# Optimization experiments

Hardware: AMD Instinct MI355X
Metric: run time of the kernel (lower is better)

The kernel has to match this reference:

```python
import jax, jax.numpy as jnp
import numpy as np

DIM = 768
H = 12
DH = DIM // H          # 64
ROPE_DIM = (DH // 6) * 6   # 60
HALF = (ROPE_DIM // 3) // 2  # 10 freqs per axis
THETA = 10000.0
EPS = 1e-6


def rmsnorm(x, w):
    xf = x.astype(jnp.float32)
    var = jnp.mean(xf * xf, axis=-1, keepdims=True)
    return (w * (xf * jax.lax.rsqrt(var + EPS))).astype(x.dtype)


def rope_angles(positions):
    # positions: [B, N, 3] -> angles [B, N, 3*HALF]
    freqs = 1.0 / (THETA ** (jnp.arange(HALF, dtype=jnp.float32) / HALF))  # [HALF]
    # [B,N,3,1] * [1,1,1,HALF] -> [B,N,3,HALF] -> concat over axis order x,y,z
    ang = positions[..., :, None] * freqs[None, None, None, :]
    return ang.reshape(*positions.shape[:2], 3 * HALF)  # [B,N,30]


def apply_rope(t, cos, sin):
    # t: [B,N,H,ROPE_DIM]; cos/sin: [B,N,1,ROPE_DIM//2]
    B, N, Hh, D = t.shape
    tf = t.astype(jnp.float32).reshape(B, N, Hh, D // 2, 2)
    te, to = tf[..., 0], tf[..., 1]
    oe = te * cos - to * sin
    oo = te * sin + to * cos
    return jnp.stack([oe, oo], axis=-1).reshape(B, N, Hh, D).astype(t.dtype)


def setup_inputs() -> dict:
    key = jax.random.key(0)
    ks = jax.random.split(key, 5)
    B, N = 2, 2048
    x = jax.random.normal(ks[0], (B, N, DIM), dtype=jnp.float32)
    positions = jax.random.uniform(ks[1], (B, N, 3), dtype=jnp.float32)
    qkv_w = jax.random.normal(ks[2], (3 * DIM, DIM), dtype=jnp.float32) * (DIM ** -0.5)
    proj_w = jax.random.normal(ks[3], (DIM, DIM), dtype=jnp.float32) * (DIM ** -0.5)
    proj_b = jnp.zeros((DIM,), dtype=jnp.float32)
    qn_w = jnp.ones((DH,), dtype=jnp.float32)
    kn_w = jnp.ones((DH,), dtype=jnp.float32)
    return {"x": x, "positions": positions, "qkv_w": qkv_w, "proj_w": proj_w,
            "proj_b": proj_b, "qn_w": qn_w, "kn_w": kn_w}


def reference(x, positions, qkv_w, proj_w, proj_b, qn_w, kn_w):
    B, N, C = x.shape
    scale = DH ** -0.5
    qkv = (x @ qkv_w.T).reshape(B, N, 3, H, DH)
    q, k, v = qkv[:, :, 0], qkv[:, :, 1], qkv[:, :, 2]  # [B,N,H,DH]
    q = rmsnorm(q, qn_w)
    k = rmsnorm(k, kn_w)
    # 3D RoPE on first ROPE_DIM channels
    ang = rope_angles(positions)                 # [B,N,30]
    cos = jnp.cos(ang)[:, :, None, :]            # [B,N,1,30]
    sin = jnp.sin(ang)[:, :, None, :]
    q = jnp.concatenate([apply_rope(q[..., :ROPE_DIM], cos, sin), q[..., ROPE_DIM:]], axis=-1)
    k = jnp.concatenate([apply_rope(k[..., :ROPE_DIM], cos, sin), k[..., ROPE_DIM:]], axis=-1)
    attn = jnp.einsum('bqhd,bkhd->bhqk', q, k) * scale  # [B,H,N,N]
    attn = jax.nn.softmax(attn, axis=-1)
    out = jnp.einsum('bhqk,bkhd->bqhd', attn, v).reshape(B, N, C)
    return out @ proj_w.T + proj_b
```

## Files before the change

### kernel.cpp

```cpp
#include <hip/hip_runtime.h>
#include <hip/hip_bf16.h>
#include <math.h>

#define DIM 768
#define NH 12
#define DH 64
#define SEQ 2048
#define BATCH 2
#define TOK (BATCH*SEQ)
#define QKVN (3*DIM)

typedef __attribute__((ext_vector_type(8))) short bf16x8;
typedef __attribute__((ext_vector_type(4))) float f32x4;
typedef __attribute__((ext_vector_type(2))) unsigned int u32x2;
typedef unsigned short u16;

#define VM0 asm volatile("s_waitcnt vmcnt(0)" ::: "memory")
#define VM3 asm volatile("s_waitcnt vmcnt(3)" ::: "memory")
#define VM4 asm volatile("s_waitcnt vmcnt(4)" ::: "memory")
#define LGKM0 asm volatile("s_waitcnt lgkmcnt(0)" ::: "memory")
#define BAR() __builtin_amdgcn_s_barrier()

__device__ inline u16 f2bf(float f) {
  union { float f; unsigned u; } v; v.f = f;
  unsigned u = v.u;
  u += 0x7fffu + ((u >> 16) & 1u);
  return (u16)(u >> 16);
}

__device__ inline int pkbf(float a, float b) {
  __hip_bfloat162 h = __float22bfloat162_rn(make_float2(a, b));
  int r; __builtin_memcpy(&r, &h, 4); return r;
}

__global__ void conv_all(const float* __restrict__ a, u16* __restrict__ ao, int na4,
                         const float* __restrict__ b, u16* __restrict__ bo, int nb4,
                         const float* __restrict__ c, u16* __restrict__ co, int nc4,
                         const float* __restrict__ pos, float2* __restrict__ tab) {
  int i4 = blockIdx.x * blockDim.x + threadIdx.x;
  const int nconv = na4 + nb4 + nc4;
  if (i4 < nconv) {
    const float* src; u16* dst; int off;
    if (i4 < na4)            { src = a; dst = ao; off = i4; }
    else if (i4 < na4 + nb4) { src = b; dst = bo; off = i4 - na4; }
    else                     { src = c; dst = co; off = i4 - na4 - nb4; }
    float4 v = ((const float4*)src)[off];
    ushort4 o;
    o.x = f2bf(v.x); o.y = f2bf(v.y); o.z = f2bf(v.z); o.w = f2bf(v.w);
    ((ushort4*)dst)[off] = o;
    return;
  }
  int e = i4 - nconv;
  if (e >= TOK * 32) return;
  int t = e >> 5, p = e & 31;
  float cs = 1.f, sn = 0.f;
  if (p < 30) {
    int axis = p / 10, fi = p % 10;
    float freq = exp2f(-(float)fi * 1.3287712379549449f);
    float ang = pos[t * 3 + axis] * freq;
    cs = cosf(ang); sn = sinf(ang);
  }
  tab[e] = make_float2(cs, sn);
}

#define GLL(g, s) __builtin_amdgcn_global_load_lds((const __attribute__((address_space(1))) void*)(g), (__attribute__((address_space(3))) void*)(s), 16, 0, 0)

__global__ __launch_bounds__(256, 4) void gemm64(
    const u16* __restrict__ A, const u16* __restrict__ W,
    float* __restrict__ C, const float* __restrict__ bias,
    int M, int Nn, int K)
{
  __shared__ u16 As[2][64 * 64];
  __shared__ u16 Bs[2][64 * 64];
  const int t = threadIdx.x;
  const int w = t >> 6, l = t & 63;
  const int lr = l & 15, lg = l >> 4;
  const int wr = w >> 1, wc = w & 1;
  const int m0 = blockIdx.x * 64;
  const int n0 = blockIdx.y * 64;
  f32x4 acc[2][2] = {};
  const int srow = t >> 3;
  const int scol = (((t & 7) ^ (srow & 7)) * 8);
  const u16* aSrc = A + (size_t)(m0 + srow) * K + scol;
  const u16* bSrc = W + (size_t)(n0 + srow) * K + scol;
  const size_t r32 = (size_t)32 * K;
  const int sw = lr & 7;
  const int NT = K / 64;

  GLL(aSrc,       &As[0][w * 512]);
  GLL(aSrc + r32, &As[0][2048 + w * 512]);
  GLL(bSrc,       &Bs[0][w * 512]);
  GLL(bSrc + r32, &Bs[0][2048 + w * 512]);

  for (int kt = 0; kt < NT; ++kt) {
    const int cur = kt & 1;
    if (kt + 1 < NT) {
      const int k0 = (kt + 1) * 64;
      GLL(aSrc + k0,       &As[cur ^ 1][w * 512]);
      GLL(aSrc + r32 + k0, &As[cur ^ 1][2048 + w * 512]);
      GLL(bSrc + k0,       &Bs[cur ^ 1][w * 512]);
      GLL(bSrc + r32 + k0, &Bs[cur ^ 1][2048 + w * 512]);
      VM4;
    } else {
      VM0;
    }
    BAR();
#pragma unroll
    for (int kk = 0; kk < 2; ++kk) {
      bf16x8 af[2], bff[2];
#pragma unroll
      for (int mi = 0; mi < 2; ++mi)
        af[mi] = *(const bf16x8*)(&As[cur][0] + (wr * 32 + mi * 16 + lr) * 64 + (((kk * 4 + lg) ^ sw) * 8));
#pragma unroll
      for (int ni = 0; ni < 2; ++ni)
        bff[ni] = *(const bf16x8*)(&Bs[cur][0] + (wc * 32 + ni * 16 + lr) * 64 + (((kk * 4 + lg) ^ sw) * 8));
#pragma unroll
      for (int mi = 0; mi < 2; ++mi)
#pragma unroll
        for (int ni = 0; ni < 2; ++ni)
          acc[mi][ni] = __builtin_amdgcn_mfma_f32_16x16x32_bf16(af[mi], bff[ni], acc[mi][ni], 0, 0, 0);
    }
    LGKM0;
    BAR();
  }

#pragma unroll
  for (int mi = 0; mi < 2; ++mi)
#pragma unroll
    for (int ni = 0; ni < 2; ++ni)
#pragma unroll
      for (int r = 0; r < 4; ++r) {
        int row = m0 + wr * 32 + mi * 16 + lg * 4 + r;
        int col = n0 + wc * 32 + ni * 16 + lr;
        C[(size_t)row * Nn + col] = acc[mi][ni][r] + bias[col];
      }
}

__global__ __launch_bounds__(512, 6) void gemm_qkv(
    const u16* __restrict__ A, const u16* __restrict__ W,
    const float* __restrict__ qn_w, const float* __restrict__ kn_w,
    const float2* __restrict__ tab,
    u16* __restrict__ Qb, u16* __restrict__ Kb, u16* __restrict__ Vtb)
{
  __shared__ u16 As[2][128 * 64];
  __shared__ u16 Bs[2][64 * 64];
  const int K = DIM;
  const int t = threadIdx.x;
  const int w = t >> 6, l = t & 63;
  const int lr = l & 15, lg = l >> 4;
  const int m0 = blockIdx.x * 128;
  const int n0 = blockIdx.y * 64;
  f32x4 acc[4] = {};
  const int srow = t >> 3;
  const int scol = (((t & 7) ^ (srow & 7)) * 8);
  const u16* aSrc = A + (size_t)(m0 + srow) * K + scol;
  const u16* bSrc = W + (size_t)(n0 + srow) * K + scol;
  const size_t r64 = (size_t)64 * K;
  const int sw = lr & 7;
  const int NT = K / 64;

  GLL(aSrc,       &As[0][w * 512]);
  GLL(aSrc + r64, &As[0][4096 + w * 512]);
  GLL(bSrc,       &Bs[0][w * 512]);

  for (int kt = 0; kt < NT; ++kt) {
    const int cur = kt & 1;
    if (kt + 1 < NT) {
      const int k0 = (kt + 1) * 64;
      GLL(aSrc + k0,       &As[cur ^ 1][w * 512]);
      GLL(aSrc + r64 + k0, &As[cur ^ 1][4096 + w * 512]);
      GLL(bSrc + k0,       &Bs[cur ^ 1][w * 512]);
      VM3;
    } else {
      VM0;
    }
    BAR();
#pragma unroll
    for (int kk = 0; kk < 2; ++kk) {
      bf16x8 af = *(const bf16x8*)(&As[cur][0] + (w * 16 + lr) * 64 + (((kk * 4 + lg) ^ sw) * 8));
      bf16x8 bff[4];
#pragma unroll
      for (int ni = 0; ni < 4; ++ni)
        bff[ni] = *(const bf16x8*)(&Bs[cur][0] + (ni * 16 + lr) * 64 + (((kk * 4 + lg) ^ sw) * 8));
#pragma unroll
      for (int ni = 0; ni < 4; ++ni)
        acc[ni] = __builtin_amdgcn_mfma_f32_16x16x32_bf16(af, bff[ni], acc[ni], 0, 0, 0);
    }
    LGKM0;
    BAR();
  }

  const int chunk = n0 >> 6;
  const int tt = chunk / 12;
  const int h  = chunk % 12;
  const int bB = m0 >> 11;
  const int bh = bB * NH + h;

  if (tt == 2) {
    const int nbase = (m0 + w * 16 + lg * 4) & 2047;
#pragma unroll
    for (int ni = 0; ni < 4; ++ni) {
      const int d = ni * 16 + lr;
      ushort4 o;
      o.x = f2bf(acc[ni][0]); o.y = f2bf(acc[ni][1]);
      o.z = f2bf(acc[ni][2]); o.w = f2bf(acc[ni][3]);
      *(ushort4*)(Vtb + ((size_t)bh * DH + d) * SEQ + nbase) = o;
    }
  } else {
    const float* wv = (tt == 0 ? qn_w : kn_w);
    const float qs = (tt == 0 ? 0.125f * 1.4426950408889634f : 1.f);
    float wgt[4];
#pragma unroll
    for (int ni = 0; ni < 4; ++ni) wgt[ni] = wv[ni * 16 + lr];
    u16* outp = (tt == 0 ? Qb : Kb) + (size_t)bh * SEQ * DH;
#pragma unroll
    for (int r = 0; r < 4; ++r) {
      float ss = 0.f;
#pragma unroll
      for (int ni = 0; ni < 4; ++ni) ss += acc[ni][r] * acc[ni][r];
      ss += __shfl_xor(ss, 1, 64);
      ss += __shfl_xor(ss, 2, 64);
      ss += __shfl_xor(ss, 4, 64);
      ss += __shfl_xor(ss, 8, 64);
      const float rms = rsqrtf(ss * (1.f / 64.f) + 1e-6f);
      const int trow = m0 + w * 16 + lg * 4 + r;
      const float2* tl = tab + trow * 32;
      u16* rowp = outp + (size_t)(trow & 2047) * DH;
#pragma unroll
      for (int ni = 0; ni < 4; ++ni) {
        const int d = ni * 16 + lr;
        float v = acc[ni][r] * rms * wgt[ni];
        float vp = __shfl_xor(v, 1, 64);
        float2 cssn = tl[ni * 8 + (lr >> 1)];
        float sgn = (d & 1) ? cssn.y : -cssn.y;
        rowp[d] = f2bf((v * cssn.x + vp * sgn) * qs);
      }
    }
  }
}

__global__ __launch_bounds__(256, 3) void attn(
    const u16* __restrict__ Qb, const u16* __restrict__ Kb,
    const u16* __restrict__ Vtb, u16* __restrict__ Ob)
{
  __shared__ u16 Ks[2][2][64 * 64];
  __shared__ u16 Vs[2][64 * 64];
  const int tid = threadIdx.x;
  const int w = tid >> 6, l = tid & 63;
  const int lr = l & 15, lg = l >> 4;
  const int qg = w & 1, half = w >> 1;
  const int wg = blockIdx.x;
  const int swz = (wg & 7) * 96 + (wg >> 3);
  const int bh = swz >> 5;
  const int q0 = (swz & 31) * 64;
  const u16* Qp = Qb + (size_t)bh * SEQ * DH;
  const u16* Kp = Kb + (size_t)bh * SEQ * DH;
  const u16* Vp = Vtb + (size_t)bh * DH * SEQ;

  const int qrA = q0 + qg * 32 + lr;
  const bf16x8 bq0a = *(const bf16x8*)(Qp + (size_t)qrA * DH + 8 * lg);
  const bf16x8 bq1a = *(const bf16x8*)(Qp + (size_t)qrA * DH + 32 + 8 * lg);
  const bf16x8 bq0b = *(const bf16x8*)(Qp + (size_t)(qrA + 16) * DH + 8 * lg);
  const bf16x8 bq1b = *(const bf16x8*)(Qp + (size_t)(qrA + 16) * DH + 32 + 8 * lg);

  const int srow = tid >> 3;
  const int sc16 = (tid & 7) ^ (srow & 7);
  const u16* kSrc = Kp + (size_t)srow * DH + sc16 * 8;
  const u16* vSrc = Vp + (size_t)srow * SEQ + sc16 * 8;

  const int frow = (lr & 3) | ((lr & 4) << 1) | ((lr & 8) >> 1);
  const int ksw = frow & 7;
  const int vsw = lr & 7;

  bf16x8 vone;
#pragma unroll
  for (int j = 0; j < 8; ++j) vone[j] = (short)0x3F80;

  f32x4 oaccA[4] = {}, oaccB[4] = {};
  f32x4 laccA = {}, laccB = {};

  GLL(kSrc,          &Ks[0][0][w * 512]);
  GLL(kSrc + 2048,   &Ks[0][0][w * 512 + 2048]);
  GLL(kSrc + 4096,   &Ks[0][1][w * 512]);
  GLL(kSrc + 6144,   &Ks[0][1][w * 512 + 2048]);
  VM0;
  BAR();
  GLL(vSrc,              &Vs[0][w * 512]);
  GLL(vSrc + 65536,      &Vs[0][w * 512 + 2048]);
  GLL(vSrc + 64,         &Vs[1][w * 512]);
  GLL(vSrc + 64 + 65536, &Vs[1][w * 512 + 2048]);
  GLL(kSrc + 8192,   &Ks[1][0][w * 512]);
  GLL(kSrc + 10240,  &Ks[1][0][w * 512 + 2048]);
  GLL(kSrc + 12288,  &Ks[1][1][w * 512]);
  GLL(kSrc + 14336,  &Ks[1][1][w * 512 + 2048]);

  for (int i = 0; i < 16; ++i) {
    const int p = i & 1;
    const u16* Kt = &Ks[p][half][0];
    const u16* Vt = &Vs[half][0];

    f32x4 paccA[4] = {}, paccB[4] = {};
    __builtin_amdgcn_s_setprio(1);
#pragma unroll
    for (int c = 0; c < 4; ++c) {
      const int rbase = (16 * c + frow) * 64;
      bf16x8 ka = *(const bf16x8*)(Kt + rbase + ((lg ^ ksw) * 8));
      bf16x8 kb = *(const bf16x8*)(Kt + rbase + (((4 + lg) ^ ksw) * 8));
      paccA[c] = __builtin_amdgcn_mfma_f32_16x16x32_bf16(ka, bq0a, paccA[c], 0, 0, 0);
      paccA[c] = __builtin_amdgcn_mfma_f32_16x16x32_bf16(kb, bq1a, paccA[c], 0, 0, 0);
      paccB[c] = __builtin_amdgcn_mfma_f32_16x16x32_bf16(ka, bq0b, paccB[c], 0, 0, 0);
      paccB[c] = __builtin_amdgcn_mfma_f32_16x16x32_bf16(kb, bq1b, paccB[c], 0, 0, 0);
    }
    __builtin_amdgcn_s_setprio(0);

    union { unsigned d[4]; bf16x8 v; } puA[2], puB[2];
#pragma unroll
    for (int g = 0; g < 2; ++g) {
      const int clo = 2 * g, chi = 2 * g + 1;
      float eA[8], eB[8];
#pragma unroll
      for (int r = 0; r < 4; ++r) {
        eA[r]     = __builtin_amdgcn_exp2f(paccA[clo][r]);
        eA[4 + r] = __builtin_amdgcn_exp2f(paccA[chi][r]);
        eB[r]     = __builtin_amdgcn_exp2f(paccB[clo][r]);
        eB[4 + r] = __builtin_amdgcn_exp2f(paccB[chi][r]);
      }
      u32x2 a0 = __builtin_amdgcn_permlane32_swap((unsigned)pkbf(eA[0], eA[1]),
                                                  (unsigned)pkbf(eA[4], eA[5]), false, false);
      u32x2 a1 = __builtin_amdgcn_permlane32_swap((unsigned)pkbf(eA[2], eA[3]),
                                                  (unsigned)pkbf(eA[6], eA[7]), false, false);
      u32x2 b0 = __builtin_amdgcn_permlane32_swap((unsigned)pkbf(eB[0], eB[1]),
                                                  (unsigned)pkbf(eB[4], eB[5]), false, false);
      u32x2 b1 = __builtin_amdgcn_permlane32_swap((unsigned)pkbf(eB[2], eB[3]),
                                                  (unsigned)pkbf(eB[6], eB[7]), false, false);
      puA[g].d[0] = a0[0]; puA[g].d[1] = a1[0]; puA[g].d[2] = a0[1]; puA[g].d[3] = a1[1];
      puB[g].d[0] = b0[0]; puB[g].d[1] = b1[0]; puB[g].d[2] = b0[1]; puB[g].d[3] = b1[1];
    }

    if (i < 15) { VM4; } else { VM0; }
    BAR();

    __builtin_amdgcn_s_setprio(1);
#pragma unroll
    for (int g = 0; g < 2; ++g) {
#pragma unroll
      for (int dt = 0; dt < 4; ++dt) {
        bf16x8 va = *(const bf16x8*)(Vt + (16 * dt + lr) * 64 + (((4 * g + lg) ^ vsw) * 8));
        oaccA[dt] = __builtin_amdgcn_mfma_f32_16x16x32_bf16(va, puA[g].v, oaccA[dt], 0, 0, 0);
        oaccB[dt] = __builtin_amdgcn_mfma_f32_16x16x32_bf16(va, puB[g].v, oaccB[dt], 0, 0, 0);
      }
      laccA = __builtin_amdgcn_mfma_f32_16x16x32_bf16(vone, puA[g].v, laccA, 0, 0, 0);
      laccB = __builtin_amdgcn_mfma_f32_16x16x32_bf16(vone, puB[g].v, laccB, 0, 0, 0);
    }
    __builtin_amdgcn_s_setprio(0);

    LGKM0;
    VM0;
    BAR();

    if (i + 1 < 16) {
      const size_t vo = (size_t)(2 * i + 2) * 64;
      GLL(vSrc + vo,              &Vs[0][w * 512]);
      GLL(vSrc + vo + 65536,      &Vs[0][w * 512 + 2048]);
      GLL(vSrc + vo + 64,         &Vs[1][w * 512]);
      GLL(vSrc + vo + 64 + 65536, &Vs[1][w * 512 + 2048]);
    }
    if (i + 2 < 16) {
      const size_t ko = (size_t)(2 * i + 4) * 4096;
      GLL(kSrc + ko,        &Ks[p][0][w * 512]);
      GLL(kSrc + ko + 2048, &Ks[p][0][w * 512 + 2048]);
      GLL(kSrc + ko + 4096, &Ks[p][1][w * 512]);
      GLL(kSrc + ko + 6144, &Ks[p][1][w * 512 + 2048]);
    }
  }

  float* scr = (float*)&Ks[0][0][0];
  const int sidA = (qg * 2 + 0) * 64 + l;
  const int sidB = (qg * 2 + 1) * 64 + l;
  if (half == 1) {
#pragma unroll
    for (int dt = 0; dt < 4; ++dt)
#pragma unroll
      for (int r = 0; r < 4; ++r) {
        scr[sidA * 17 + dt * 4 + r] = oaccA[dt][r];
        scr[sidB * 17 + dt * 4 + r] = oaccB[dt][r];
      }
    scr[sidA * 17 + 16] = laccA[0];
    scr[sidB * 17 + 16] = laccB[0];
  }
  __syncthreads();
  if (half == 1) return;
#pragma unroll
  for (int dt = 0; dt < 4; ++dt)
#pragma unroll
    for (int r = 0; r < 4; ++r) {
      oaccA[dt][r] += scr[sidA * 17 + dt * 4 + r];
      oaccB[dt][r] += scr[sidB * 17 + dt * 4 + r];
    }
  const float invA = 1.f / (laccA[0] + scr[sidA * 17 + 16]);
  const float invB = 1.f / (laccB[0] + scr[sidB * 17 + 16]);

  const int b = bh / NH, h = bh % NH;
  const int qA = q0 + qg * 32 + lr;
  size_t obA = (size_t)(b * SEQ + qA) * DIM + h * DH + 4 * lg;
  size_t obB = (size_t)(b * SEQ + qA + 16) * DIM + h * DH + 4 * lg;
#pragma unroll
  for (int dt = 0; dt < 4; ++dt) {
    ushort4 oA, oB;
    oA.x = f2bf(oaccA[dt][0] * invA); oA.y = f2bf(oaccA[dt][1] * invA);
    oA.z = f2bf(oaccA[dt][2] * invA); oA.w = f2bf(oaccA[dt][3] * invA);
    oB.x = f2bf(oaccB[dt][0] * invB); oB.y = f2bf(oaccB[dt][1] * invB);
    oB.z = f2bf(oaccB[dt][2] * invB); oB.w = f2bf(oaccB[dt][3] * invB);
    *(ushort4*)(Ob + obA + 16 * dt) = oA;
    *(ushort4*)(Ob + obB + 16 * dt) = oB;
  }
}

extern "C" void kernel_launch(void* const* d_in, const int* in_sizes, int n_in,
                              void* d_out, int out_size, void* d_ws, size_t ws_size,
                              hipStream_t stream) {
  const float* x      = (const float*)d_in[0];
  const float* pos    = (const float*)d_in[1];
  const float* qkv_w  = (const float*)d_in[2];
  const float* proj_w = (const float*)d_in[3];
  const float* proj_b = (const float*)d_in[4];
  const float* qn_w   = (const float*)d_in[5];
  const float* kn_w   = (const float*)d_in[6];
  char* ws = (char*)d_ws;
  u16*    xb    = (u16*)(ws + 0);
  u16*    wqkv  = (u16*)(ws + 6291456);
  u16*    wproj = (u16*)(ws + 9830400);
  float2* tab   = (float2*)(ws + 11010048);
  u16*    Qb    = (u16*)(ws + 12058624);
  u16*    Kb    = (u16*)(ws + 18350080);
  u16*    Vtb   = (u16*)(ws + 24641536);
  u16*    Ob    = (u16*)(ws + 30932992);
  float* out = (float*)d_out;

  const int na4 = TOK * DIM / 4, nb4 = QKVN * DIM / 4, nc4 = DIM * DIM / 4;
  const int ntot = na4 + nb4 + nc4 + TOK * 32;
  conv_all<<<(ntot + 255) / 256, 256, 0, stream>>>(
      x, xb, na4, qkv_w, wqkv, nb4, proj_w, wproj, nc4, pos, tab);

  dim3 g1(TOK / 128, QKVN / 64);
  gemm_qkv<<<g1, 512, 0, stream>>>(xb, wqkv, qn_w, kn_w, tab, Qb, Kb, Vtb);

  attn<<<SEQ / 64 * BATCH * NH, 256, 0, stream>>>(Qb, Kb, Vtb, Ob);

  dim3 g3(TOK / 64, DIM / 64);
  gemm64<<<g3, 256, 0, stream>>>(Ob, wproj, out, proj_b, TOK, DIM, DIM);
}
```

Before: 87.12 us.

## Fuse fp32-to-bf16 conversion and RoPE table into GEMM loaders

Removes the separate conversion kernel. The QKV and projection GEMMs now load fp32 inputs and weights directly through registers, convert them to bf16 and write them into swizzled LDS, which replaces the async global-to-LDS path. The RoPE cos/sin values are computed inline in the QKV epilogue from the positions instead of read from a precomputed table. This saves one launch and the bf16 round trip through memory, but doubles the bytes each GEMM reads, re-converts weights in every block, and adds transcendental work to the epilogue.

```diff
diff --git a/kernel.cpp b/kernel.cpp
--- a/kernel.cpp
+++ b/kernel.cpp
@@ -16,7 +16,6 @@
 typedef unsigned short u16;
 
 #define VM0 asm volatile("s_waitcnt vmcnt(0)" ::: "memory")
-#define VM3 asm volatile("s_waitcnt vmcnt(3)" ::: "memory")
 #define VM4 asm volatile("s_waitcnt vmcnt(4)" ::: "memory")
 #define LGKM0 asm volatile("s_waitcnt lgkmcnt(0)" ::: "memory")
 #define BAR() __builtin_amdgcn_s_barrier()
@@ -33,40 +32,17 @@
   int r; __builtin_memcpy(&r, &h, 4); return r;
 }
 
-__global__ void conv_all(const float* __restrict__ a, u16* __restrict__ ao, int na4,
-                         const float* __restrict__ b, u16* __restrict__ bo, int nb4,
-                         const float* __restrict__ c, u16* __restrict__ co, int nc4,
-                         const float* __restrict__ pos, float2* __restrict__ tab) {
-  int i4 = blockIdx.x * blockDim.x + threadIdx.x;
-  const int nconv = na4 + nb4 + nc4;
-  if (i4 < nconv) {
-    const float* src; u16* dst; int off;
-    if (i4 < na4)            { src = a; dst = ao; off = i4; }
-    else if (i4 < na4 + nb4) { src = b; dst = bo; off = i4 - na4; }
-    else                     { src = c; dst = co; off = i4 - na4 - nb4; }
-    float4 v = ((const float4*)src)[off];
-    ushort4 o;
-    o.x = f2bf(v.x); o.y = f2bf(v.y); o.z = f2bf(v.z); o.w = f2bf(v.w);
-    ((ushort4*)dst)[off] = o;
-    return;
-  }
-  int e = i4 - nconv;
-  if (e >= TOK * 32) return;
-  int t = e >> 5, p = e & 31;
-  float cs = 1.f, sn = 0.f;
-  if (p < 30) {
-    int axis = p / 10, fi = p % 10;
-    float freq = exp2f(-(float)fi * 1.3287712379549449f);
-    float ang = pos[t * 3 + axis] * freq;
-    cs = cosf(ang); sn = sinf(ang);
-  }
-  tab[e] = make_float2(cs, sn);
+__device__ inline void wr8(u16* dst, float4 x, float4 y) {
+  union { u16 u[8]; bf16x8 v; } o;
+  o.u[0] = f2bf(x.x); o.u[1] = f2bf(x.y); o.u[2] = f2bf(x.z); o.u[3] = f2bf(x.w);
+  o.u[4] = f2bf(y.x); o.u[5] = f2bf(y.y); o.u[6] = f2bf(y.z); o.u[7] = f2bf(y.w);
+  *(bf16x8*)dst = o.v;
 }
 
 #define GLL(g, s) __builtin_amdgcn_global_load_lds((const __attribute__((address_space(1))) void*)(g), (__attribute__((address_space(3))) void*)(s), 16, 0, 0)
 
 __global__ __launch_bounds__(256, 4) void gemm64(
-    const u16* __restrict__ A, const u16* __restrict__ W,
+    const u16* __restrict__ A, const float* __restrict__ W,
     float* __restrict__ C, const float* __restrict__ bias,
     int M, int Nn, int K)
 {
@@ -80,31 +56,42 @@
   const int n0 = blockIdx.y * 64;
   f32x4 acc[2][2] = {};
   const int srow = t >> 3;
-  const int scol = (((t & 7) ^ (srow & 7)) * 8);
-  const u16* aSrc = A + (size_t)(m0 + srow) * K + scol;
-  const u16* bSrc = W + (size_t)(n0 + srow) * K + scol;
+  const int sc16 = (t & 7) ^ (srow & 7);
+  const u16* aSrc = A + (size_t)(m0 + srow) * K + sc16 * 8;
   const size_t r32 = (size_t)32 * K;
+  const int rw = t >> 2, jw = (t & 3) * 2;
+  const float* bSrc = W + (size_t)(n0 + rw) * K + jw * 8;
+  const int wof0 = rw * 64 + ((jw ^ (rw & 7)) * 8);
+  const int wof1 = rw * 64 + (((jw + 1) ^ (rw & 7)) * 8);
   const int sw = lr & 7;
   const int NT = K / 64;
 
   GLL(aSrc,       &As[0][w * 512]);
   GLL(aSrc + r32, &As[0][2048 + w * 512]);
-  GLL(bSrc,       &Bs[0][w * 512]);
-  GLL(bSrc + r32, &Bs[0][2048 + w * 512]);
+  {
+    float4 b0 = *(const float4*)(bSrc);
+    float4 b1 = *(const float4*)(bSrc + 4);
+    float4 b2 = *(const float4*)(bSrc + 8);
+    float4 b3 = *(const float4*)(bSrc + 12);
+    wr8(&Bs[0][wof0], b0, b1);
+    wr8(&Bs[0][wof1], b2, b3);
+  }
+  VM0; LGKM0; BAR();
 
   for (int kt = 0; kt < NT; ++kt) {
     const int cur = kt & 1;
-    if (kt + 1 < NT) {
+    const bool pre = (kt + 1 < NT);
+    float4 b0, b1, b2, b3;
+    if (pre) {
       const int k0 = (kt + 1) * 64;
       GLL(aSrc + k0,       &As[cur ^ 1][w * 512]);
       GLL(aSrc + r32 + k0, &As[cur ^ 1][2048 + w * 512]);
-      GLL(bSrc + k0,       &Bs[cur ^ 1][w * 512]);
-      GLL(bSrc + r32 + k0, &Bs[cur ^ 1][2048 + w * 512]);
-      VM4;
-    } else {
-      VM0;
-    }
-    BAR();
+      const float* bp = bSrc + k0;
+      b0 = *(const float4*)(bp);
+      b1 = *(const float4*)(bp + 4);
+      b2 = *(const float4*)(bp + 8);
+      b3 = *(const float4*)(bp + 12);
+    }
 #pragma unroll
     for (int kk = 0; kk < 2; ++kk) {
       bf16x8 af[2], bff[2];
@@ -120,7 +107,12 @@
         for (int ni = 0; ni < 2; ++ni)
           acc[mi][ni] = __builtin_amdgcn_mfma_f32_16x16x32_bf16(af[mi], bff[ni], acc[mi][ni], 0, 0, 0);
     }
+    if (pre) {
+      wr8(&Bs[cur ^ 1][wof0], b0, b1);
+      wr8(&Bs[cur ^ 1][wof1], b2, b3);
+    }
     LGKM0;
+    VM0;
     BAR();
   }
 
@@ -137,9 +129,9 @@
 }
 
 __global__ __launch_bounds__(512, 6) void gemm_qkv(
-    const u16* __restrict__ A, const u16* __restrict__ W,
+    const float* __restrict__ X, const float* __restrict__ Wq,
     const float* __restrict__ qn_w, const float* __restrict__ kn_w,
-    const float2* __restrict__ tab,
+    const float* __restrict__ pos,
     u16* __restrict__ Qb, u16* __restrict__ Kb, u16* __restrict__ Vtb)
 {
   __shared__ u16 As[2][128 * 64];
@@ -151,30 +143,43 @@
   const int m0 = blockIdx.x * 128;
   const int n0 = blockIdx.y * 64;
   f32x4 acc[4] = {};
-  const int srow = t >> 3;
-  const int scol = (((t & 7) ^ (srow & 7)) * 8);
-  const u16* aSrc = A + (size_t)(m0 + srow) * K + scol;
-  const u16* bSrc = W + (size_t)(n0 + srow) * K + scol;
-  const size_t r64 = (size_t)64 * K;
+  const int ra = t >> 2, ja = (t & 3) * 2;
+  const float* aSrc = X + (size_t)(m0 + ra) * K + ja * 8;
+  const int aof0 = ra * 64 + ((ja ^ (ra & 7)) * 8);
+  const int aof1 = ra * 64 + (((ja + 1) ^ (ra & 7)) * 8);
+  const int rb = t >> 3, jb = t & 7;
+  const float* bSrc = Wq + (size_t)(n0 + rb) * K + jb * 8;
+  const int bof = rb * 64 + ((jb ^ (rb & 7)) * 8);
   const int sw = lr & 7;
   const int NT = K / 64;
 
-  GLL(aSrc,       &As[0][w * 512]);
-  GLL(aSrc + r64, &As[0][4096 + w * 512]);
-  GLL(bSrc,       &Bs[0][w * 512]);
+  {
+    float4 a0 = *(const float4*)(aSrc);
+    float4 a1 = *(const float4*)(aSrc + 4);
+    float4 a2 = *(const float4*)(aSrc + 8);
+    float4 a3 = *(const float4*)(aSrc + 12);
+    float4 b0 = *(const float4*)(bSrc);
+    float4 b1 = *(const float4*)(bSrc + 4);
+    wr8(&As[0][aof0], a0, a1);
+    wr8(&As[0][aof1], a2, a3);
+    wr8(&Bs[0][bof], b0, b1);
+  }
+  LGKM0; BAR();
 
   for (int kt = 0; kt < NT; ++kt) {
     const int cur = kt & 1;
-    if (kt + 1 < NT) {
-      const int k0 = (kt + 1) * 64;
-      GLL(aSrc + k0,       &As[cur ^ 1][w * 512]);
-      GLL(aSrc + r64 + k0, &As[cur ^ 1][4096 + w * 512]);
-      GLL(bSrc + k0,       &Bs[cur ^ 1][w * 512]);
-      VM3;
-    } else {
-      VM0;
-    }
-    BAR();
+    const bool pre = (kt + 1 < NT);
+    float4 a0, a1, a2, a3, b0, b1;
+    if (pre) {
+      const float* ap = aSrc + (kt + 1) * 64;
+      const float* bp = bSrc + (kt + 1) * 64;
+      a0 = *(const float4*)(ap);
+      a1 = *(const float4*)(ap + 4);
+      a2 = *(const float4*)(ap + 8);
+      a3 = *(const float4*)(ap + 12);
+      b0 = *(const float4*)(bp);
+      b1 = *(const float4*)(bp + 4);
+    }
 #pragma unroll
     for (int kk = 0; kk < 2; ++kk) {
       bf16x8 af = *(const bf16x8*)(&As[cur][0] + (w * 16 + lr) * 64 + (((kk * 4 + lg) ^ sw) * 8));
@@ -185,6 +190,11 @@
 #pragma unroll
       for (int ni = 0; ni < 4; ++ni)
         acc[ni] = __builtin_amdgcn_mfma_f32_16x16x32_bf16(af, bff[ni], acc[ni], 0, 0, 0);
+    }
+    if (pre) {
+      wr8(&As[cur ^ 1][aof0], a0, a1);
+      wr8(&As[cur ^ 1][aof1], a2, a3);
+      wr8(&Bs[cur ^ 1][bof], b0, b1);
     }
     LGKM0;
     BAR();
@@ -209,9 +219,17 @@
   } else {
     const float* wv = (tt == 0 ? qn_w : kn_w);
     const float qs = (tt == 0 ? 0.125f * 1.4426950408889634f : 1.f);
-    float wgt[4];
-#pragma unroll
-    for (int ni = 0; ni < 4; ++ni) wgt[ni] = wv[ni * 16 + lr];
+    float wgt[4], freqv[4];
+    int axv[4]; bool actv[4];
+#pragma unroll
+    for (int ni = 0; ni < 4; ++ni) {
+      wgt[ni] = wv[ni * 16 + lr];
+      const int pidx = ni * 8 + (lr >> 1);
+      actv[ni] = (pidx < 30);
+      const int axis = pidx / 10, fi = pidx % 10;
+      axv[ni] = axis;
+      freqv[ni] = exp2f(-(float)fi * 1.3287712379549449f);
+    }
     u16* outp = (tt == 0 ? Qb : Kb) + (size_t)bh * SEQ * DH;
 #pragma unroll
     for (int r = 0; r < 4; ++r) {
@@ -224,16 +242,21 @@
       ss += __shfl_xor(ss, 8, 64);
       const float rms = rsqrtf(ss * (1.f / 64.f) + 1e-6f);
       const int trow = m0 + w * 16 + lg * 4 + r;
-      const float2* tl = tab + trow * 32;
+      const float pa = pos[trow * 3], pb = pos[trow * 3 + 1], pc = pos[trow * 3 + 2];
       u16* rowp = outp + (size_t)(trow & 2047) * DH;
 #pragma unroll
       for (int ni = 0; ni < 4; ++ni) {
         const int d = ni * 16 + lr;
+        float cs = 1.f, sn = 0.f;
+        if (actv[ni]) {
+          const float pv = (axv[ni] == 0) ? pa : ((axv[ni] == 1) ? pb : pc);
+          const float ang = pv * freqv[ni];
+          cs = cosf(ang); sn = sinf(ang);
+        }
         float v = acc[ni][r] * rms * wgt[ni];
         float vp = __shfl_xor(v, 1, 64);
-        float2 cssn = tl[ni * 8 + (lr >> 1)];
-        float sgn = (d & 1) ? cssn.y : -cssn.y;
-        rowp[d] = f2bf((v * cssn.x + vp * sgn) * qs);
+        float sgn = (d & 1) ? sn : -sn;
+        rowp[d] = f2bf((v * cs + vp * sgn) * qs);
       }
     }
   }
@@ -427,26 +450,17 @@
   const float* qn_w   = (const float*)d_in[5];
   const float* kn_w   = (const float*)d_in[6];
   char* ws = (char*)d_ws;
-  u16*    xb    = (u16*)(ws + 0);
-  u16*    wqkv  = (u16*)(ws + 6291456);
-  u16*    wproj = (u16*)(ws + 9830400);
-  float2* tab   = (float2*)(ws + 11010048);
-  u16*    Qb    = (u16*)(ws + 12058624);
-  u16*    Kb    = (u16*)(ws + 18350080);
-  u16*    Vtb   = (u16*)(ws + 24641536);
-  u16*    Ob    = (u16*)(ws + 30932992);
+  u16* Qb  = (u16*)(ws + 0);
+  u16* Kb  = (u16*)(ws + 6291456);
+  u16* Vtb = (u16*)(ws + 12582912);
+  u16* Ob  = (u16*)(ws + 18874368);
   float* out = (float*)d_out;
 
-  const int na4 = TOK * DIM / 4, nb4 = QKVN * DIM / 4, nc4 = DIM * DIM / 4;
-  const int ntot = na4 + nb4 + nc4 + TOK * 32;
-  conv_all<<<(ntot + 255) / 256, 256, 0, stream>>>(
-      x, xb, na4, qkv_w, wqkv, nb4, proj_w, wproj, nc4, pos, tab);
-
   dim3 g1(TOK / 128, QKVN / 64);
-  gemm_qkv<<<g1, 512, 0, stream>>>(xb, wqkv, qn_w, kn_w, tab, Qb, Kb, Vtb);
+  gemm_qkv<<<g1, 512, 0, stream>>>(x, qkv_w, qn_w, kn_w, pos, Qb, Kb, Vtb);
 
   attn<<<SEQ / 64 * BATCH * NH, 256, 0, stream>>>(Qb, Kb, Vtb, Ob);
 
   dim3 g3(TOK / 64, DIM / 64);
-  gemm64<<<g3, 256, 0, stream>>>(Ob, wproj, out, proj_b, TOK, DIM, DIM);
-}
+  gemm64<<<g3, 256, 0, stream>>>(Ob, proj_w, out, proj_b, TOK, DIM, DIM);
+}
```

Result: slower. 107.5 us (+23.4%).

## Give each attention wave 16 queries over all keys instead of split-key halves

Applied to the files above, without the earlier changes.

The attention kernel changes its work split. Before, each wave handled 32 queries over half of every key/value tile, and the two halves were reduced through shared memory at the end. Now each wave owns 16 query rows over the full key range, using a simple two-stage double buffer of 64-key K/V tiles with one barrier per iteration. This removes the cross-wave reduction and cuts shared memory from 48KB to 32KB, and launch bounds rise from 3 to 5 blocks for higher occupancy. In exchange, each K/V fragment read from shared memory now feeds half as many MFMAs, and the loop runs twice as many iterations and barriers.

```diff
diff --git a/kernel.cpp b/kernel.cpp
--- a/kernel.cpp
+++ b/kernel.cpp
@@ -239,16 +239,15 @@
   }
 }
 
-__global__ __launch_bounds__(256, 3) void attn(
+__global__ __launch_bounds__(256, 5) void attn(
     const u16* __restrict__ Qb, const u16* __restrict__ Kb,
     const u16* __restrict__ Vtb, u16* __restrict__ Ob)
 {
-  __shared__ u16 Ks[2][2][64 * 64];
-  __shared__ u16 Vs[2][64 * 64];
+  __shared__ u16 Kd[2][64 * 64];
+  __shared__ u16 Vd[2][64 * 64];
   const int tid = threadIdx.x;
   const int w = tid >> 6, l = tid & 63;
   const int lr = l & 15, lg = l >> 4;
-  const int qg = w & 1, half = w >> 1;
   const int wg = blockIdx.x;
   const int swz = (wg & 7) * 96 + (wg >> 3);
   const int bh = swz >> 5;
@@ -257,11 +256,9 @@
   const u16* Kp = Kb + (size_t)bh * SEQ * DH;
   const u16* Vp = Vtb + (size_t)bh * DH * SEQ;
 
-  const int qrA = q0 + qg * 32 + lr;
-  const bf16x8 bq0a = *(const bf16x8*)(Qp + (size_t)qrA * DH + 8 * lg);
-  const bf16x8 bq1a = *(const bf16x8*)(Qp + (size_t)qrA * DH + 32 + 8 * lg);
-  const bf16x8 bq0b = *(const bf16x8*)(Qp + (size_t)(qrA + 16) * DH + 8 * lg);
-  const bf16x8 bq1b = *(const bf16x8*)(Qp + (size_t)(qrA + 16) * DH + 32 + 8 * lg);
+  const int qrow = q0 + w * 16 + lr;
+  const bf16x8 bq0 = *(const bf16x8*)(Qp + (size_t)qrow * DH + 8 * lg);
+  const bf16x8 bq1 = *(const bf16x8*)(Qp + (size_t)qrow * DH + 32 + 8 * lg);
 
   const int srow = tid >> 3;
   const int sc16 = (tid & 7) ^ (srow & 7);
@@ -276,69 +273,57 @@
 #pragma unroll
   for (int j = 0; j < 8; ++j) vone[j] = (short)0x3F80;
 
-  f32x4 oaccA[4] = {}, oaccB[4] = {};
-  f32x4 laccA = {}, laccB = {};
-
-  GLL(kSrc,          &Ks[0][0][w * 512]);
-  GLL(kSrc + 2048,   &Ks[0][0][w * 512 + 2048]);
-  GLL(kSrc + 4096,   &Ks[0][1][w * 512]);
-  GLL(kSrc + 6144,   &Ks[0][1][w * 512 + 2048]);
+  f32x4 oacc[4] = {};
+  f32x4 lacc = {};
+
+  GLL(kSrc,         &Kd[0][w * 512]);
+  GLL(kSrc + 2048,  &Kd[0][w * 512 + 2048]);
+  GLL(vSrc,         &Vd[0][w * 512]);
+  GLL(vSrc + 65536, &Vd[0][w * 512 + 2048]);
   VM0;
   BAR();
-  GLL(vSrc,              &Vs[0][w * 512]);
-  GLL(vSrc + 65536,      &Vs[0][w * 512 + 2048]);
-  GLL(vSrc + 64,         &Vs[1][w * 512]);
-  GLL(vSrc + 64 + 65536, &Vs[1][w * 512 + 2048]);
-  GLL(kSrc + 8192,   &Ks[1][0][w * 512]);
-  GLL(kSrc + 10240,  &Ks[1][0][w * 512 + 2048]);
-  GLL(kSrc + 12288,  &Ks[1][1][w * 512]);
-  GLL(kSrc + 14336,  &Ks[1][1][w * 512 + 2048]);
-
-  for (int i = 0; i < 16; ++i) {
-    const int p = i & 1;
-    const u16* Kt = &Ks[p][half][0];
-    const u16* Vt = &Vs[half][0];
-
-    f32x4 paccA[4] = {}, paccB[4] = {};
+
+  for (int i = 0; i < 32; ++i) {
+    const int cur = i & 1;
+    if (i + 1 < 32) {
+      const size_t ko = (size_t)(i + 1) * 4096;
+      const size_t vo = (size_t)(i + 1) * 64;
+      GLL(kSrc + ko,         &Kd[cur ^ 1][w * 512]);
+      GLL(kSrc + ko + 2048,  &Kd[cur ^ 1][w * 512 + 2048]);
+      GLL(vSrc + vo,         &Vd[cur ^ 1][w * 512]);
+      GLL(vSrc + vo + 65536, &Vd[cur ^ 1][w * 512 + 2048]);
+    }
+    const u16* Kt = &Kd[cur][0];
+    const u16* Vt = &Vd[cur][0];
+
+    f32x4 pacc[4] = {};
     __builtin_amdgcn_s_setprio(1);
 #pragma unroll
     for (int c = 0; c < 4; ++c) {
       const int rbase = (16 * c + frow) * 64;
       bf16x8 ka = *(const bf16x8*)(Kt + rbase + ((lg ^ ksw) * 8));
       bf16x8 kb = *(const bf16x8*)(Kt + rbase + (((4 + lg) ^ ksw) * 8));
-      paccA[c] = __builtin_amdgcn_mfma_f32_16x16x32_bf16(ka, bq0a, paccA[c], 0, 0, 0);
-      paccA[c] = __builtin_amdgcn_mfma_f32_16x16x32_bf16(kb, bq1a, paccA[c], 0, 0, 0);
-      paccB[c] = __builtin_amdgcn_mfma_f32_16x16x32_bf16(ka, bq0b, paccB[c], 0, 0, 0);
-      paccB[c] = __builtin_amdgcn_mfma_f32_16x16x32_bf16(kb, bq1b, paccB[c], 0, 0, 0);
+      pacc[c] = __builtin_amdgcn_mfma_f32_16x16x32_bf16(ka, bq0, pacc[c], 0, 0, 0);
+      pacc[c] = __builtin_amdgcn_mfma_f32_16x16x32_bf16(kb, bq1, pacc[c], 0, 0, 0);
     }
     __builtin_amdgcn_s_setprio(0);
 
-    union { unsigned d[4]; bf16x8 v; } puA[2], puB[2];
+    union { unsigned d[4]; bf16x8 v; } pu[2];
 #pragma unroll
     for (int g = 0; g < 2; ++g) {
       const int clo = 2 * g, chi = 2 * g + 1;
-      float eA[8], eB[8];
+      float e[8];
 #pragma unroll
       for (int r = 0; r < 4; ++r) {
-        eA[r]     = __builtin_amdgcn_exp2f(paccA[clo][r]);
-        eA[4 + r] = __builtin_amdgcn_exp2f(paccA[chi][r]);
-        eB[r]     = __builtin_amdgcn_exp2f(paccB[clo][r]);
-        eB[4 + r] = __builtin_amdgcn_exp2f(paccB[chi][r]);
+        e[r]     = __builtin_amdgcn_exp2f(pacc[clo][r]);
+        e[4 + r] = __builtin_amdgcn_exp2f(pacc[chi][r]);
       }
-      u32x2 a0 = __builtin_amdgcn_permlane32_swap((unsigned)pkbf(eA[0], eA[1]),
-                                                  (unsigned)pkbf(eA[4], eA[5]), false, false);
-      u32x2 a1 = __builtin_amdgcn_permlane32_swap((unsigned)pkbf(eA[2], eA[3]),
-                                                  (unsigned)pkbf(eA[6], eA[7]), false, false);
-      u32x2 b0 = __builtin_amdgcn_permlane32_swap((unsigned)pkbf(eB[0], eB[1]),
-                                                  (unsigned)pkbf(eB[4], eB[5]), false, false);
-      u32x2 b1 = __builtin_amdgcn_permlane32_swap((unsigned)pkbf(eB[2], eB[3]),
-                                                  (unsigned)pkbf(eB[6], eB[7]), false, false);
-      puA[g].d[0] = a0[0]; puA[g].d[1] = a1[0]; puA[g].d[2] = a0[1]; puA[g].d[3] = a1[1];
-      puB[g].d[0] = b0[0]; puB[g].d[1] = b1[0]; puB[g].d[2] = b0[1]; puB[g].d[3] = b1[1];
-    }
-
-    if (i < 15) { VM4; } else { VM0; }
-    BAR();
+      u32x2 a0 = __builtin_amdgcn_permlane32_swap((unsigned)pkbf(e[0], e[1]),
+                                                  (unsigned)pkbf(e[4], e[5]), false, false);
+      u32x2 a1 = __builtin_amdgcn_permlane32_swap((unsigned)pkbf(e[2], e[3]),
+                                                  (unsigned)pkbf(e[6], e[7]), false, false);
+      pu[g].d[0] = a0[0]; pu[g].d[1] = a1[0]; pu[g].d[2] = a0[1]; pu[g].d[3] = a1[1];
+    }
 
     __builtin_amdgcn_s_setprio(1);
 #pragma unroll
@@ -346,73 +331,31 @@
 #pragma unroll
       for (int dt = 0; dt < 4; ++dt) {
         bf16x8 va = *(const bf16x8*)(Vt + (16 * dt + lr) * 64 + (((4 * g + lg) ^ vsw) * 8));
-        oaccA[dt] = __builtin_amdgcn_mfma_f32_16x16x32_bf16(va, puA[g].v, oaccA[dt], 0, 0, 0);
-        oaccB[dt] = __builtin_amdgcn_mfma_f32_16x16x32_bf16(va, puB[g].v, oaccB[dt], 0, 0, 0);
+        oacc[dt] = __builtin_amdgcn_mfma_f32_16x16x32_bf16(va, pu[g].v, oacc[dt], 0, 0, 0);
       }
-      laccA = __builtin_amdgcn_mfma_f32_16x16x32_bf16(vone, puA[g].v, laccA, 0, 0, 0);
-      laccB = __builtin_amdgcn_mfma_f32_16x16x32_bf16(vone, puB[g].v, laccB, 0, 0, 0);
+      lacc = __builtin_amdgcn_mfma_f32_16x16x32_bf16(vone, pu[g].v, lacc, 0, 0, 0);
     }
     __builtin_amdgcn_s_setprio(0);
 
-    LGKM0;
-    VM0;
-    BAR();
-
-    if (i + 1 < 16) {
-      const size_t vo = (size_t)(2 * i + 2) * 64;
-      GLL(vSrc + vo,              &Vs[0][w * 512]);
-      GLL(vSrc + vo + 65536,      &Vs[0][w * 512 + 2048]);
-      GLL(vSrc + vo + 64,         &Vs[1][w * 512]);
-      GLL(vSrc + vo + 64 + 65536, &Vs[1][w * 512 + 2048]);
-    }
-    if (i + 2 < 16) {
-      const size_t ko = (size_t)(2 * i + 4) * 4096;
-      GLL(kSrc + ko,        &Ks[p][0][w * 512]);
-      GLL(kSrc + ko + 2048, &Ks[p][0][w * 512 + 2048]);
-      GLL(kSrc + ko + 4096, &Ks[p][1][w * 512]);
-      GLL(kSrc + ko + 6144, &Ks[p][1][w * 512 + 2048]);
-    }
-  }
-
-  float* scr = (float*)&Ks[0][0][0];
-  const int sidA = (qg * 2 + 0) * 64 + l;
-  const int sidB = (qg * 2 + 1) * 64 + l;
-  if (half == 1) {
-#pragma unroll
-    for (int dt = 0; dt < 4; ++dt)
-#pragma unroll
-      for (int r = 0; r < 4; ++r) {
-        scr[sidA * 17 + dt * 4 + r] = oaccA[dt][r];
-        scr[sidB * 17 + dt * 4 + r] = oaccB[dt][r];
-      }
-    scr[sidA * 17 + 16] = laccA[0];
-    scr[sidB * 17 + 16] = laccB[0];
-  }
-  __syncthreads();
-  if (half == 1) return;
-#pragma unroll
-  for (int dt = 0; dt < 4; ++dt)
-#pragma unroll
-    for (int r = 0; r < 4; ++r) {
-      oaccA[dt][r] += scr[sidA * 17 + dt * 4 + r];
-      oaccB[dt][r] += scr[sidB * 17 + dt * 4 + r];
-    }
-  const float invA = 1.f / (laccA[0] + scr[sidA * 17 + 16]);
-  const float invB = 1.f / (laccB[0] + scr[sidB * 17 + 16]);
-
+    if (i + 1 < 32) {
+      LGKM0;
+      VM0;
+      BAR();
+    }
+  }
+
+  const float inv = 1.f / lacc[0];
   const int b = bh / NH, h = bh % NH;
-  const int qA = q0 + qg * 32 + lr;
-  size_t obA = (size_t)(b * SEQ + qA) * DIM + h * DH + 4 * lg;
-  size_t obB = (size_t)(b * SEQ + qA + 16) * DIM + h * DH + 4 * lg;
+  const int q = q0 + w * 16 + lr;
+  size_t obase = (size_t)(b * SEQ + q) * DIM + h * DH + 4 * lg;
 #pragma unroll
   for (int dt = 0; dt < 4; ++dt) {
-    ushort4 oA, oB;
-    oA.x = f2bf(oaccA[dt][0] * invA); oA.y = f2bf(oaccA[dt][1] * invA);
-    oA.z = f2bf(oaccA[dt][2] * invA); oA.w = f2bf(oaccA[dt][3] * invA);
-    oB.x = f2bf(oaccB[dt][0] * invB); oB.y = f2bf(oaccB[dt][1] * invB);
-    oB.z = f2bf(oaccB[dt][2] * invB); oB.w = f2bf(oaccB[dt][3] * invB);
-    *(ushort4*)(Ob + obA + 16 * dt) = oA;
-    *(ushort4*)(Ob + obB + 16 * dt) = oB;
+    ushort4 o;
+    o.x = f2bf(oacc[dt][0] * inv);
+    o.y = f2bf(oacc[dt][1] * inv);
+    o.z = f2bf(oacc[dt][2] * inv);
+    o.w = f2bf(oacc[dt][3] * inv);
+    *(ushort4*)(Ob + obase + 16 * dt) = o;
   }
 }
 
```

After: 90.69 us. +4.1%, slower.
